# Kernel optimization log

Hardware: AMD Instinct MI355X
Metric: run time of the kernel (lower is better)

The kernel has to match this reference:

```python
import jax, jax.numpy as jnp
import numpy as np

LN_EPS = 1e-5


def _layernorm(x, w, b):
    mu = jnp.mean(x, axis=-1, keepdims=True)
    var = jnp.mean((x - mu) ** 2, axis=-1, keepdims=True)
    return (x - mu) * jax.lax.rsqrt(var + LN_EPS) * w + b


def setup_inputs() -> dict:
    key = jax.random.key(0)
    n, d = 512, 256
    ks = jax.random.split(key, 12)
    s = 1.0 / np.sqrt(d)
    inp = {
        "h": jax.random.normal(ks[0], (n, d), dtype=jnp.float32),
        "e": jax.random.normal(ks[1], (n, n, d), dtype=jnp.float32),
        "t_emb": jax.random.normal(ks[2], (d,), dtype=jnp.float32),
        "W1": jax.random.uniform(ks[3], (d, d), jnp.float32, -s, s),
        "W2": jax.random.uniform(ks[4], (d, d), jnp.float32, -s, s),
        "W3": jax.random.uniform(ks[5], (d, d), jnp.float32, -s, s),
        "W_t": jax.random.uniform(ks[6], (d, d), jnp.float32, -s, s),
        "W4": jax.random.uniform(ks[7], (d, d), jnp.float32, -s, s),
        "W5": jax.random.uniform(ks[8], (d, d), jnp.float32, -s, s),
        "gate_w": jax.random.uniform(ks[9], (d, 1), jnp.float32, -s, s),
        "gate_b": jax.random.uniform(ks[10], (1,), jnp.float32, -s, s),
        "ln_e_w": jnp.ones((d,), jnp.float32),
        "ln_e_b": jnp.zeros((d,), jnp.float32),
        "ln_h_w": jnp.ones((d,), jnp.float32),
        "ln_h_b": jnp.zeros((d,), jnp.float32),
    }
    return inp


def reference(h, e, t_emb, W1, W2, W3, W_t, W4, W5, gate_w, gate_b,
              ln_e_w, ln_e_b, ln_h_w, ln_h_b):
    # nn.Linear applies x @ W.T (no bias except gate)
    t_bias = t_emb @ W_t.T                      # (d,)
    hi = (h @ W1.T)[:, None, :]                 # (n,1,d)
    hj = (h @ W2.T)[None, :, :]                 # (1,n,d)
    pre = hi + hj + jnp.einsum('ijd,kd->ijk', e, W3) + t_bias  # (n,n,d)
    e_new = jax.nn.relu(_layernorm(pre, ln_e_w, ln_e_b))       # (n,n,d)
    logits = e_new @ gate_w + gate_b            # (n,n,1)
    eta = jax.nn.softmax(logits, axis=1)        # softmax over j (dim=1)
    agg = jnp.einsum('ijk,ijd,kd->ik', eta * 1.0, e_new, W5) if False else \
          jnp.sum(eta * jnp.einsum('ijd,kd->ijk', e_new, W5), axis=1)  # (n,d)
    h_new = h + jax.nn.relu(_layernorm(h @ W4.T + agg, ln_h_w, ln_h_b))
    return (h_new, e_new)
```

## Files before the change

kernel.cpp:

```cpp
#include <hip/hip_runtime.h>

#define NN 512
#define DD 256

typedef float f32x4 __attribute__((ext_vector_type(4)));
typedef short s16x8 __attribute__((ext_vector_type(8)));

__device__ __forceinline__ unsigned short f2bf(float f) {
    unsigned u = __float_as_uint(f);
    u += 0x7fffu + ((u >> 16) & 1u);
    return (unsigned short)(u >> 16);
}

__global__ __launch_bounds__(256) void k1_pre(
    const float* __restrict__ h,  const float* __restrict__ W1,
    const float* __restrict__ W2, const float* __restrict__ W4,
    const float* __restrict__ t_emb, const float* __restrict__ W_t,
    const float* __restrict__ W3,
    float* __restrict__ hW1, float* __restrict__ hW2, float* __restrict__ hW4,
    float* __restrict__ tbias, unsigned short* __restrict__ w3b)
{
    __shared__ float xs[8][DD];
    const int b = blockIdx.x;
    const int t = threadIdx.x;
    if (b < 64) {
        #pragma unroll
        for (int r = 0; r < 8; ++r) xs[r][t] = h[(size_t)(b * 8 + r) * DD + t];
        __syncthreads();
        float a1[8], a2[8], a4[8];
        #pragma unroll
        for (int r = 0; r < 8; ++r) { a1[r] = 0.f; a2[r] = 0.f; a4[r] = 0.f; }
        for (int d = 0; d < DD; ++d) {
            const float w1 = W1[(size_t)t * DD + d];
            const float w2 = W2[(size_t)t * DD + d];
            const float w4 = W4[(size_t)t * DD + d];
            #pragma unroll
            for (int r = 0; r < 8; ++r) {
                const float x = xs[r][d];
                a1[r] = fmaf(x, w1, a1[r]);
                a2[r] = fmaf(x, w2, a2[r]);
                a4[r] = fmaf(x, w4, a4[r]);
            }
        }
        #pragma unroll
        for (int r = 0; r < 8; ++r) {
            const size_t o = (size_t)(b * 8 + r) * DD + t;
            hW1[o] = a1[r]; hW2[o] = a2[r]; hW4[o] = a4[r];
        }
    } else {
        xs[0][t] = t_emb[t];
        __syncthreads();
        float a = 0.f;
        for (int d = 0; d < DD; ++d) a = fmaf(xs[0][d], W_t[(size_t)t * DD + d], a);
        tbias[t] = a;
        for (int c = t; c < DD * DD / 4; c += 256) {
            const f32x4 v = *reinterpret_cast<const f32x4*>(W3 + (size_t)c * 4);
            const unsigned lo = ((unsigned)f2bf(v[1]) << 16) | f2bf(v[0]);
            const unsigned hi = ((unsigned)f2bf(v[3]) << 16) | f2bf(v[2]);
            *reinterpret_cast<uint2*>(w3b + (size_t)c * 4) = make_uint2(lo, hi);
        }
    }
}

__global__ __launch_bounds__(256) void k2_big(
    const float* __restrict__ e,
    const unsigned short* __restrict__ w3b,
    const float* __restrict__ hW1, const float* __restrict__ hW2,
    const float* __restrict__ tbias,
    const float* __restrict__ gate_w, const float* __restrict__ gate_b,
    const float* __restrict__ ln_e_w, const float* __restrict__ ln_e_b,
    float* __restrict__ out_e, float* __restrict__ logits)
{
    const int blk = blockIdx.x;
    const int row_base = blk * 64;
    const int i = row_base >> 9;
    const int tid = threadIdx.x;
    const int w = tid >> 6;
    const int l = tid & 63;
    const int l15 = l & 15;
    const int lg = l >> 4;

    __shared__ __align__(16) unsigned char sA[64 * 256 * 2];
    __shared__ float s_part[64][4][2];
    __shared__ float s_mu[64];
    __shared__ float s_rs[64];
    __shared__ float s_glog[64][4];

    {
        const float* src = e + (size_t)row_base * DD;
        #pragma unroll
        for (int s = 0; s < 16; ++s) {
            const int flat = s * 256 + tid;
            const int r = flat >> 6;
            const int c4 = (flat & 63) * 4;
            const f32x4 v = *reinterpret_cast<const f32x4*>(src + (size_t)flat * 4);
            const unsigned lo = ((unsigned)f2bf(v[1]) << 16) | f2bf(v[0]);
            const unsigned hi = ((unsigned)f2bf(v[3]) << 16) | f2bf(v[2]);
            const unsigned byte = ((unsigned)(r * 512 + c4 * 2)) ^ ((unsigned)(r & 7) << 4);
            *reinterpret_cast<uint2*>(sA + byte) = make_uint2(lo, hi);
        }
    }
    __syncthreads();

    f32x4 acc[4][4];
    #pragma unroll
    for (int m = 0; m < 4; ++m)
        #pragma unroll
        for (int n = 0; n < 4; ++n)
            acc[m][n] = (f32x4){0.f, 0.f, 0.f, 0.f};

    const unsigned aswz = ((unsigned)(l15 & 7) << 4);
    for (int kk = 0; kk < 8; ++kk) {
        s16x8 afr[4];
        #pragma unroll
        for (int m = 0; m < 4; ++m) {
            const unsigned byte = ((unsigned)((m * 16 + l15) * 512 + kk * 64 + lg * 16)) ^ aswz;
            afr[m] = *reinterpret_cast<const s16x8*>(sA + byte);
        }
        #pragma unroll
        for (int n = 0; n < 4; ++n) {
            const int col = w * 64 + n * 16 + l15;
            const s16x8 bfr = *reinterpret_cast<const s16x8*>(w3b + (size_t)col * DD + kk * 32 + lg * 8);
            #pragma unroll
            for (int m = 0; m < 4; ++m)
                acc[m][n] = __builtin_amdgcn_mfma_f32_16x16x32_bf16(afr[m], bfr, acc[m][n], 0, 0, 0);
        }
    }

    float hw1c[4], tbc[4], lnwc[4], lnbc[4], gwc[4];
    #pragma unroll
    for (int n = 0; n < 4; ++n) {
        const int col = w * 64 + n * 16 + l15;
        hw1c[n] = hW1[(size_t)i * DD + col];
        tbc[n]  = tbias[col];
        lnwc[n] = ln_e_w[col];
        lnbc[n] = ln_e_b[col];
        gwc[n]  = gate_w[col];
    }

    #pragma unroll
    for (int m = 0; m < 4; ++m) {
        #pragma unroll
        for (int q = 0; q < 4; ++q) {
            const int r = m * 16 + lg * 4 + q;
            const int j = (row_base + r) & 511;
            float s1 = 0.f, s2 = 0.f;
            #pragma unroll
            for (int n = 0; n < 4; ++n) {
                const int col = w * 64 + n * 16 + l15;
                float v = acc[m][n][q] + hw1c[n] + tbc[n] + hW2[(size_t)j * DD + col];
                acc[m][n][q] = v;
                s1 += v;
                s2 += v * v;
            }
            #pragma unroll
            for (int s = 1; s < 16; s <<= 1) {
                s1 += __shfl_xor(s1, s, 64);
                s2 += __shfl_xor(s2, s, 64);
            }
            if (l15 == 0) { s_part[r][w][0] = s1; s_part[r][w][1] = s2; }
        }
    }
    __syncthreads();
    if (tid < 64) {
        float S1 = 0.f, S2 = 0.f;
        #pragma unroll
        for (int ww = 0; ww < 4; ++ww) { S1 += s_part[tid][ww][0]; S2 += s_part[tid][ww][1]; }
        const float mu = S1 * (1.f / 256.f);
        const float var = S2 * (1.f / 256.f) - mu * mu;
        s_mu[tid] = mu;
        s_rs[tid] = rsqrtf(var + 1e-5f);
    }
    __syncthreads();

    #pragma unroll
    for (int m = 0; m < 4; ++m) {
        #pragma unroll
        for (int q = 0; q < 4; ++q) {
            const int r = m * 16 + lg * 4 + q;
            const float mu = s_mu[r];
            const float rs = s_rs[r];
            const size_t rowg = (size_t)(row_base + r);
            float gl = 0.f;
            #pragma unroll
            for (int n = 0; n < 4; ++n) {
                const int col = w * 64 + n * 16 + l15;
                float v = (acc[m][n][q] - mu) * rs * lnwc[n] + lnbc[n];
                v = fmaxf(v, 0.f);
                out_e[rowg * DD + col] = v;
                gl = fmaf(v, gwc[n], gl);
            }
            #pragma unroll
            for (int s = 1; s < 16; s <<= 1) gl += __shfl_xor(gl, s, 64);
            if (l15 == 0) s_glog[r][w] = gl;
        }
    }
    __syncthreads();
    if (tid < 64) {
        float g = gate_b[0];
        #pragma unroll
        for (int ww = 0; ww < 4; ++ww) g += s_glog[tid][ww];
        logits[(size_t)row_base + tid] = g;
    }
}

__global__ __launch_bounds__(256) void k3_soft(
    const float* __restrict__ logits, const float* __restrict__ out_e,
    float* __restrict__ weighted)
{
    const int i = blockIdx.x;
    const int t = threadIdx.x;
    const int w = t >> 6;
    const int l = t & 63;
    __shared__ float seta[NN];
    __shared__ float red[256];
    __shared__ float red2[4][DD];

    const float l0 = logits[(size_t)i * NN + t];
    const float l1 = logits[(size_t)i * NN + 256 + t];

    red[t] = fmaxf(l0, l1);
    __syncthreads();
    for (int s = 128; s > 0; s >>= 1) {
        if (t < s) red[t] = fmaxf(red[t], red[t + s]);
        __syncthreads();
    }
    const float mx = red[0];
    __syncthreads();

    const float e0 = expf(l0 - mx);
    const float e1 = expf(l1 - mx);
    red[t] = e0 + e1;
    __syncthreads();
    for (int s = 128; s > 0; s >>= 1) {
        if (t < s) red[t] += red[t + s];
        __syncthreads();
    }
    const float inv = 1.f / red[0];
    seta[t] = e0 * inv;
    seta[256 + t] = e1 * inv;
    __syncthreads();

    const float* base = out_e + (size_t)i * NN * DD;
    f32x4 a0 = (f32x4){0.f, 0.f, 0.f, 0.f};
    f32x4 a1v = (f32x4){0.f, 0.f, 0.f, 0.f};
    for (int j0 = 0; j0 < NN; j0 += 8) {
        const int ja = j0 + w;
        const int jb = j0 + 4 + w;
        const float ea = seta[ja];
        const float eb = seta[jb];
        const f32x4 va = *reinterpret_cast<const f32x4*>(base + (size_t)ja * DD + l * 4);
        const f32x4 vb = *reinterpret_cast<const f32x4*>(base + (size_t)jb * DD + l * 4);
        #pragma unroll
        for (int q = 0; q < 4; ++q) {
            a0[q] = fmaf(ea, va[q], a0[q]);
            a1v[q] = fmaf(eb, vb[q], a1v[q]);
        }
    }
    #pragma unroll
    for (int q = 0; q < 4; ++q) a0[q] += a1v[q];
    *reinterpret_cast<f32x4*>(&red2[w][l * 4]) = a0;
    __syncthreads();
    weighted[(size_t)i * DD + t] = red2[0][t] + red2[1][t] + red2[2][t] + red2[3][t];
}

__global__ __launch_bounds__(256) void k4_final(
    const float* __restrict__ weighted, const float* __restrict__ W5,
    const float* __restrict__ hW4, const float* __restrict__ h,
    const float* __restrict__ ln_h_w, const float* __restrict__ ln_h_b,
    float* __restrict__ out_h)
{
    const int i = blockIdx.x;
    const int k = threadIdx.x;
    __shared__ float xs[DD];
    __shared__ float red[256];

    xs[k] = weighted[(size_t)i * DD + k];
    __syncthreads();
    float a = 0.f;
    for (int d = 0; d < DD; ++d) a = fmaf(xs[d], W5[(size_t)k * DD + d], a);
    const float p = hW4[(size_t)i * DD + k] + a;

    red[k] = p;
    __syncthreads();
    for (int s = 128; s > 0; s >>= 1) {
        if (k < s) red[k] += red[k + s];
        __syncthreads();
    }
    const float mu = red[0] * (1.f / 256.f);
    __syncthreads();
    const float d0 = p - mu;
    red[k] = d0 * d0;
    __syncthreads();
    for (int s = 128; s > 0; s >>= 1) {
        if (k < s) red[k] += red[k + s];
        __syncthreads();
    }
    const float rs = rsqrtf(red[0] * (1.f / 256.f) + 1e-5f);
    float v = d0 * rs * ln_h_w[k] + ln_h_b[k];
    v = fmaxf(v, 0.f);
    out_h[(size_t)i * DD + k] = h[(size_t)i * DD + k] + v;
}

extern "C" void kernel_launch(void* const* d_in, const int* in_sizes, int n_in,
                              void* d_out, int out_size, void* d_ws, size_t ws_size,
                              hipStream_t stream)
{
    const float* h      = (const float*)d_in[0];
    const float* e      = (const float*)d_in[1];
    const float* t_emb  = (const float*)d_in[2];
    const float* W1     = (const float*)d_in[3];
    const float* W2     = (const float*)d_in[4];
    const float* W3     = (const float*)d_in[5];
    const float* W_t    = (const float*)d_in[6];
    const float* W4     = (const float*)d_in[7];
    const float* W5     = (const float*)d_in[8];
    const float* gate_w = (const float*)d_in[9];
    const float* gate_b = (const float*)d_in[10];
    const float* ln_e_w = (const float*)d_in[11];
    const float* ln_e_b = (const float*)d_in[12];
    const float* ln_h_w = (const float*)d_in[13];
    const float* ln_h_b = (const float*)d_in[14];

    float* out_h = (float*)d_out;
    float* out_e = out_h + NN * DD;

    float* wsf      = (float*)d_ws;
    float* hW1      = wsf;
    float* hW2      = hW1 + NN * DD;
    float* hW4      = hW2 + NN * DD;
    float* tbias    = hW4 + NN * DD;
    float* logits   = tbias + DD;
    float* weighted = logits + NN * NN;
    unsigned short* w3b = (unsigned short*)(weighted + NN * DD);

    k1_pre<<<65, 256, 0, stream>>>(h, W1, W2, W4, t_emb, W_t, W3,
                                   hW1, hW2, hW4, tbias, w3b);
    k2_big<<<4096, 256, 0, stream>>>(e, w3b, hW1, hW2, tbias, gate_w, gate_b,
                                     ln_e_w, ln_e_b, out_e, logits);
    k3_soft<<<512, 256, 0, stream>>>(logits, out_e, weighted);
    k4_final<<<512, 256, 0, stream>>>(weighted, W5, hW4, h, ln_h_w, ln_h_b, out_h);
}
```

Before: 326.1 us.

## Give each wave full rows in k2 to drop LDS staging and block syncs

The main edge kernel now gives each wave 16 complete rows across all 256 output columns. A operands are loaded from global straight into registers as bf16, and the LayerNorm and gate-logit reductions are done entirely with intra-wave shuffles. This removes the shared-memory A tile and the cross-wave partial-sum exchanges with their barriers, and adds a launch-bounds occupancy hint. The t_emb bias is folded into the hW1 precompute, so k2 reads one fewer vector. In exchange each wave now reads all of W3 (256x256 bf16) from global/L2 rather than a quarter of it, and register pressure rises with 16 accumulator tiles plus 8 A fragments.

```diff
diff --git a/kernel.cpp b/kernel.cpp
--- a/kernel.cpp
+++ b/kernel.cpp
@@ -17,23 +17,27 @@
     const float* __restrict__ W2, const float* __restrict__ W4,
     const float* __restrict__ t_emb, const float* __restrict__ W_t,
     const float* __restrict__ W3,
-    float* __restrict__ hW1, float* __restrict__ hW2, float* __restrict__ hW4,
-    float* __restrict__ tbias, unsigned short* __restrict__ w3b)
+    float* __restrict__ hb, float* __restrict__ hW2, float* __restrict__ hW4,
+    unsigned short* __restrict__ w3b)
 {
     __shared__ float xs[8][DD];
+    __shared__ float st[DD];
     const int b = blockIdx.x;
     const int t = threadIdx.x;
     if (b < 64) {
         #pragma unroll
         for (int r = 0; r < 8; ++r) xs[r][t] = h[(size_t)(b * 8 + r) * DD + t];
+        st[t] = t_emb[t];
         __syncthreads();
         float a1[8], a2[8], a4[8];
         #pragma unroll
         for (int r = 0; r < 8; ++r) { a1[r] = 0.f; a2[r] = 0.f; a4[r] = 0.f; }
+        float tb = 0.f;
         for (int d = 0; d < DD; ++d) {
             const float w1 = W1[(size_t)t * DD + d];
             const float w2 = W2[(size_t)t * DD + d];
             const float w4 = W4[(size_t)t * DD + d];
+            tb = fmaf(st[d], W_t[(size_t)t * DD + d], tb);
             #pragma unroll
             for (int r = 0; r < 8; ++r) {
                 const float x = xs[r][d];
@@ -45,14 +49,9 @@
         #pragma unroll
         for (int r = 0; r < 8; ++r) {
             const size_t o = (size_t)(b * 8 + r) * DD + t;
-            hW1[o] = a1[r]; hW2[o] = a2[r]; hW4[o] = a4[r];
+            hb[o] = a1[r] + tb; hW2[o] = a2[r]; hW4[o] = a4[r];
         }
     } else {
-        xs[0][t] = t_emb[t];
-        __syncthreads();
-        float a = 0.f;
-        for (int d = 0; d < DD; ++d) a = fmaf(xs[0][d], W_t[(size_t)t * DD + d], a);
-        tbias[t] = a;
         for (int c = t; c < DD * DD / 4; c += 256) {
             const f32x4 v = *reinterpret_cast<const f32x4*>(W3 + (size_t)c * 4);
             const unsigned lo = ((unsigned)f2bf(v[1]) << 16) | f2bf(v[0]);
@@ -62,145 +61,99 @@
     }
 }
 
-__global__ __launch_bounds__(256) void k2_big(
+__global__ __launch_bounds__(256, 3) void k2_big(
     const float* __restrict__ e,
     const unsigned short* __restrict__ w3b,
-    const float* __restrict__ hW1, const float* __restrict__ hW2,
-    const float* __restrict__ tbias,
+    const float* __restrict__ hb, const float* __restrict__ hW2,
     const float* __restrict__ gate_w, const float* __restrict__ gate_b,
     const float* __restrict__ ln_e_w, const float* __restrict__ ln_e_b,
     float* __restrict__ out_e, float* __restrict__ logits)
 {
-    const int blk = blockIdx.x;
-    const int row_base = blk * 64;
+    const int row_base = blockIdx.x * 64;
     const int i = row_base >> 9;
     const int tid = threadIdx.x;
     const int w = tid >> 6;
     const int l = tid & 63;
     const int l15 = l & 15;
     const int lg = l >> 4;
-
-    __shared__ __align__(16) unsigned char sA[64 * 256 * 2];
-    __shared__ float s_part[64][4][2];
-    __shared__ float s_mu[64];
-    __shared__ float s_rs[64];
-    __shared__ float s_glog[64][4];
-
-    {
-        const float* src = e + (size_t)row_base * DD;
-        #pragma unroll
-        for (int s = 0; s < 16; ++s) {
-            const int flat = s * 256 + tid;
-            const int r = flat >> 6;
-            const int c4 = (flat & 63) * 4;
-            const f32x4 v = *reinterpret_cast<const f32x4*>(src + (size_t)flat * 4);
-            const unsigned lo = ((unsigned)f2bf(v[1]) << 16) | f2bf(v[0]);
-            const unsigned hi = ((unsigned)f2bf(v[3]) << 16) | f2bf(v[2]);
-            const unsigned byte = ((unsigned)(r * 512 + c4 * 2)) ^ ((unsigned)(r & 7) << 4);
-            *reinterpret_cast<uint2*>(sA + byte) = make_uint2(lo, hi);
-        }
-    }
-    __syncthreads();
-
-    f32x4 acc[4][4];
-    #pragma unroll
-    for (int m = 0; m < 4; ++m)
-        #pragma unroll
-        for (int n = 0; n < 4; ++n)
-            acc[m][n] = (f32x4){0.f, 0.f, 0.f, 0.f};
-
-    const unsigned aswz = ((unsigned)(l15 & 7) << 4);
+    const int g0 = row_base + w * 16;
+
+    const float* arow = e + (size_t)(g0 + l15) * DD + lg * 8;
+    s16x8 abf[8];
+    #pragma unroll
     for (int kk = 0; kk < 8; ++kk) {
-        s16x8 afr[4];
-        #pragma unroll
-        for (int m = 0; m < 4; ++m) {
-            const unsigned byte = ((unsigned)((m * 16 + l15) * 512 + kk * 64 + lg * 16)) ^ aswz;
-            afr[m] = *reinterpret_cast<const s16x8*>(sA + byte);
-        }
-        #pragma unroll
-        for (int n = 0; n < 4; ++n) {
-            const int col = w * 64 + n * 16 + l15;
-            const s16x8 bfr = *reinterpret_cast<const s16x8*>(w3b + (size_t)col * DD + kk * 32 + lg * 8);
-            #pragma unroll
-            for (int m = 0; m < 4; ++m)
-                acc[m][n] = __builtin_amdgcn_mfma_f32_16x16x32_bf16(afr[m], bfr, acc[m][n], 0, 0, 0);
-        }
-    }
-
-    float hw1c[4], tbc[4], lnwc[4], lnbc[4], gwc[4];
-    #pragma unroll
-    for (int n = 0; n < 4; ++n) {
-        const int col = w * 64 + n * 16 + l15;
-        hw1c[n] = hW1[(size_t)i * DD + col];
-        tbc[n]  = tbias[col];
-        lnwc[n] = ln_e_w[col];
-        lnbc[n] = ln_e_b[col];
-        gwc[n]  = gate_w[col];
-    }
-
-    #pragma unroll
-    for (int m = 0; m < 4; ++m) {
+        const f32x4 v0 = *reinterpret_cast<const f32x4*>(arow + kk * 32);
+        const f32x4 v1 = *reinterpret_cast<const f32x4*>(arow + kk * 32 + 4);
+        s16x8 a;
+        a[0] = (short)f2bf(v0[0]); a[1] = (short)f2bf(v0[1]);
+        a[2] = (short)f2bf(v0[2]); a[3] = (short)f2bf(v0[3]);
+        a[4] = (short)f2bf(v1[0]); a[5] = (short)f2bf(v1[1]);
+        a[6] = (short)f2bf(v1[2]); a[7] = (short)f2bf(v1[3]);
+        abf[kk] = a;
+    }
+
+    f32x4 acc[16];
+    #pragma unroll
+    for (int n = 0; n < 16; ++n) acc[n] = (f32x4){0.f, 0.f, 0.f, 0.f};
+
+    const unsigned short* bp = w3b + (size_t)l15 * DD + lg * 8;
+    #pragma unroll
+    for (int kk = 0; kk < 8; ++kk) {
+        #pragma unroll
+        for (int n = 0; n < 16; ++n) {
+            const s16x8 bfr = *reinterpret_cast<const s16x8*>(bp + (size_t)n * 16 * DD + kk * 32);
+            acc[n] = __builtin_amdgcn_mfma_f32_16x16x32_bf16(abf[kk], bfr, acc[n], 0, 0, 0);
+        }
+    }
+
+    float hbn[16];
+    #pragma unroll
+    for (int n = 0; n < 16; ++n) hbn[n] = hb[(size_t)i * DD + n * 16 + l15];
+
+    float mu4[4], rs4[4];
+    #pragma unroll
+    for (int q = 0; q < 4; ++q) {
+        const int jrow = (g0 + lg * 4 + q) & 511;
+        const float* h2p = hW2 + (size_t)jrow * DD + l15;
+        float s1 = 0.f, s2 = 0.f;
+        #pragma unroll
+        for (int n = 0; n < 16; ++n) {
+            float v = acc[n][q] + hbn[n] + h2p[n * 16];
+            acc[n][q] = v;
+            s1 += v;
+            s2 = fmaf(v, v, s2);
+        }
+        #pragma unroll
+        for (int s = 1; s < 16; s <<= 1) {
+            s1 += __shfl_xor(s1, s, 64);
+            s2 += __shfl_xor(s2, s, 64);
+        }
+        const float mu = s1 * (1.f / 256.f);
+        mu4[q] = mu;
+        rs4[q] = rsqrtf(s2 * (1.f / 256.f) - mu * mu + 1e-5f);
+    }
+
+    float gl[4] = {0.f, 0.f, 0.f, 0.f};
+    #pragma unroll
+    for (int n = 0; n < 16; ++n) {
+        const int col = n * 16 + l15;
+        const float lw = ln_e_w[col];
+        const float lb = ln_e_b[col];
+        const float gw = gate_w[col];
         #pragma unroll
         for (int q = 0; q < 4; ++q) {
-            const int r = m * 16 + lg * 4 + q;
-            const int j = (row_base + r) & 511;
-            float s1 = 0.f, s2 = 0.f;
-            #pragma unroll
-            for (int n = 0; n < 4; ++n) {
-                const int col = w * 64 + n * 16 + l15;
-                float v = acc[m][n][q] + hw1c[n] + tbc[n] + hW2[(size_t)j * DD + col];
-                acc[m][n][q] = v;
-                s1 += v;
-                s2 += v * v;
-            }
-            #pragma unroll
-            for (int s = 1; s < 16; s <<= 1) {
-                s1 += __shfl_xor(s1, s, 64);
-                s2 += __shfl_xor(s2, s, 64);
-            }
-            if (l15 == 0) { s_part[r][w][0] = s1; s_part[r][w][1] = s2; }
-        }
-    }
-    __syncthreads();
-    if (tid < 64) {
-        float S1 = 0.f, S2 = 0.f;
-        #pragma unroll
-        for (int ww = 0; ww < 4; ++ww) { S1 += s_part[tid][ww][0]; S2 += s_part[tid][ww][1]; }
-        const float mu = S1 * (1.f / 256.f);
-        const float var = S2 * (1.f / 256.f) - mu * mu;
-        s_mu[tid] = mu;
-        s_rs[tid] = rsqrtf(var + 1e-5f);
-    }
-    __syncthreads();
-
-    #pragma unroll
-    for (int m = 0; m < 4; ++m) {
-        #pragma unroll
-        for (int q = 0; q < 4; ++q) {
-            const int r = m * 16 + lg * 4 + q;
-            const float mu = s_mu[r];
-            const float rs = s_rs[r];
-            const size_t rowg = (size_t)(row_base + r);
-            float gl = 0.f;
-            #pragma unroll
-            for (int n = 0; n < 4; ++n) {
-                const int col = w * 64 + n * 16 + l15;
-                float v = (acc[m][n][q] - mu) * rs * lnwc[n] + lnbc[n];
-                v = fmaxf(v, 0.f);
-                out_e[rowg * DD + col] = v;
-                gl = fmaf(v, gwc[n], gl);
-            }
-            #pragma unroll
-            for (int s = 1; s < 16; s <<= 1) gl += __shfl_xor(gl, s, 64);
-            if (l15 == 0) s_glog[r][w] = gl;
-        }
-    }
-    __syncthreads();
-    if (tid < 64) {
-        float g = gate_b[0];
-        #pragma unroll
-        for (int ww = 0; ww < 4; ++ww) g += s_glog[tid][ww];
-        logits[(size_t)row_base + tid] = g;
+            float v = (acc[n][q] - mu4[q]) * rs4[q] * lw + lb;
+            v = fmaxf(v, 0.f);
+            out_e[(size_t)(g0 + lg * 4 + q) * DD + col] = v;
+            gl[q] = fmaf(v, gw, gl[q]);
+        }
+    }
+    const float gb = gate_b[0];
+    #pragma unroll
+    for (int q = 0; q < 4; ++q) {
+        #pragma unroll
+        for (int s = 1; s < 16; s <<= 1) gl[q] += __shfl_xor(gl[q], s, 64);
+        if (l15 == 0) logits[(size_t)(g0 + lg * 4 + q)] = gl[q] + gb;
     }
 }
 
@@ -326,17 +279,16 @@
     float* out_e = out_h + NN * DD;
 
     float* wsf      = (float*)d_ws;
-    float* hW1      = wsf;
-    float* hW2      = hW1 + NN * DD;
+    float* hb       = wsf;
+    float* hW2      = hb + NN * DD;
     float* hW4      = hW2 + NN * DD;
-    float* tbias    = hW4 + NN * DD;
-    float* logits   = tbias + DD;
+    float* logits   = hW4 + NN * DD;
     float* weighted = logits + NN * NN;
     unsigned short* w3b = (unsigned short*)(weighted + NN * DD);
 
     k1_pre<<<65, 256, 0, stream>>>(h, W1, W2, W4, t_emb, W_t, W3,
-                                   hW1, hW2, hW4, tbias, w3b);
-    k2_big<<<4096, 256, 0, stream>>>(e, w3b, hW1, hW2, tbias, gate_w, gate_b,
+                                   hb, hW2, hW4, w3b);
+    k2_big<<<4096, 256, 0, stream>>>(e, w3b, hb, hW2, gate_w, gate_b,
                                      ln_e_w, ln_e_b, out_e, logits);
     k3_soft<<<512, 256, 0, stream>>>(logits, out_e, weighted);
     k4_final<<<512, 256, 0, stream>>>(weighted, W5, hW4, h, ln_h_w, ln_h_b, out_h);
```

Result: slower. 453.0 us (+38.9%).

## Halve k2 row tile, prefetch B fragments, fold time bias into hW1

Applied to the files above, without the earlier changes.

The main edge kernel now handles 32 rows per block instead of 64, launching twice as many blocks with half the shared memory and accumulator registers, which should raise occupancy. Global loads of e are issued into registers before the W3 fragments are fetched, and W3 fragments are double-buffered across the k loop so the next step's loads overlap the MFMAs. The time-embedding bias is folded into hW1 in the first kernel, removing one workspace array and one load per column. The cost is that each block reuses its W3 fragments over fewer rows, so more W3 traffic per row.

```diff
diff --git a/kernel.cpp b/kernel.cpp
--- a/kernel.cpp
+++ b/kernel.cpp
@@ -17,23 +17,27 @@
     const float* __restrict__ W2, const float* __restrict__ W4,
     const float* __restrict__ t_emb, const float* __restrict__ W_t,
     const float* __restrict__ W3,
-    float* __restrict__ hW1, float* __restrict__ hW2, float* __restrict__ hW4,
-    float* __restrict__ tbias, unsigned short* __restrict__ w3b)
+    float* __restrict__ hb, float* __restrict__ hW2, float* __restrict__ hW4,
+    unsigned short* __restrict__ w3b)
 {
     __shared__ float xs[8][DD];
+    __shared__ float st[DD];
     const int b = blockIdx.x;
     const int t = threadIdx.x;
     if (b < 64) {
         #pragma unroll
         for (int r = 0; r < 8; ++r) xs[r][t] = h[(size_t)(b * 8 + r) * DD + t];
+        st[t] = t_emb[t];
         __syncthreads();
         float a1[8], a2[8], a4[8];
         #pragma unroll
         for (int r = 0; r < 8; ++r) { a1[r] = 0.f; a2[r] = 0.f; a4[r] = 0.f; }
+        float tb = 0.f;
         for (int d = 0; d < DD; ++d) {
             const float w1 = W1[(size_t)t * DD + d];
             const float w2 = W2[(size_t)t * DD + d];
             const float w4 = W4[(size_t)t * DD + d];
+            tb = fmaf(st[d], W_t[(size_t)t * DD + d], tb);
             #pragma unroll
             for (int r = 0; r < 8; ++r) {
                 const float x = xs[r][d];
@@ -45,14 +49,9 @@
         #pragma unroll
         for (int r = 0; r < 8; ++r) {
             const size_t o = (size_t)(b * 8 + r) * DD + t;
-            hW1[o] = a1[r]; hW2[o] = a2[r]; hW4[o] = a4[r];
+            hb[o] = a1[r] + tb; hW2[o] = a2[r]; hW4[o] = a4[r];
         }
     } else {
-        xs[0][t] = t_emb[t];
-        __syncthreads();
-        float a = 0.f;
-        for (int d = 0; d < DD; ++d) a = fmaf(xs[0][d], W_t[(size_t)t * DD + d], a);
-        tbias[t] = a;
         for (int c = t; c < DD * DD / 4; c += 256) {
             const f32x4 v = *reinterpret_cast<const f32x4*>(W3 + (size_t)c * 4);
             const unsigned lo = ((unsigned)f2bf(v[1]) << 16) | f2bf(v[0]);
@@ -65,14 +64,12 @@
 __global__ __launch_bounds__(256) void k2_big(
     const float* __restrict__ e,
     const unsigned short* __restrict__ w3b,
-    const float* __restrict__ hW1, const float* __restrict__ hW2,
-    const float* __restrict__ tbias,
+    const float* __restrict__ hb, const float* __restrict__ hW2,
     const float* __restrict__ gate_w, const float* __restrict__ gate_b,
     const float* __restrict__ ln_e_w, const float* __restrict__ ln_e_b,
     float* __restrict__ out_e, float* __restrict__ logits)
 {
-    const int blk = blockIdx.x;
-    const int row_base = blk * 64;
+    const int row_base = blockIdx.x * 32;
     const int i = row_base >> 9;
     const int tid = threadIdx.x;
     const int w = tid >> 6;
@@ -80,78 +77,94 @@
     const int l15 = l & 15;
     const int lg = l >> 4;
 
-    __shared__ __align__(16) unsigned char sA[64 * 256 * 2];
-    __shared__ float s_part[64][4][2];
-    __shared__ float s_mu[64];
-    __shared__ float s_rs[64];
-    __shared__ float s_glog[64][4];
-
-    {
-        const float* src = e + (size_t)row_base * DD;
-        #pragma unroll
-        for (int s = 0; s < 16; ++s) {
-            const int flat = s * 256 + tid;
-            const int r = flat >> 6;
-            const int c4 = (flat & 63) * 4;
-            const f32x4 v = *reinterpret_cast<const f32x4*>(src + (size_t)flat * 4);
-            const unsigned lo = ((unsigned)f2bf(v[1]) << 16) | f2bf(v[0]);
-            const unsigned hi = ((unsigned)f2bf(v[3]) << 16) | f2bf(v[2]);
-            const unsigned byte = ((unsigned)(r * 512 + c4 * 2)) ^ ((unsigned)(r & 7) << 4);
-            *reinterpret_cast<uint2*>(sA + byte) = make_uint2(lo, hi);
-        }
-    }
-    __syncthreads();
-
-    f32x4 acc[4][4];
-    #pragma unroll
-    for (int m = 0; m < 4; ++m)
+    __shared__ __align__(16) unsigned char sA[32 * 256 * 2];
+    __shared__ float s_part[32][4][2];
+    __shared__ float s_mu[32];
+    __shared__ float s_rs[32];
+    __shared__ float s_glog[32][4];
+
+    const float* src = e + (size_t)row_base * DD;
+    f32x4 av[8];
+    #pragma unroll
+    for (int s = 0; s < 8; ++s)
+        av[s] = *reinterpret_cast<const f32x4*>(src + (size_t)(s * 256 + tid) * 4);
+
+    const unsigned short* bp = w3b + (size_t)(w * 64 + l15) * DD + lg * 8;
+    s16x8 bcur[4];
+    #pragma unroll
+    for (int n = 0; n < 4; ++n)
+        bcur[n] = *reinterpret_cast<const s16x8*>(bp + (size_t)n * 16 * DD);
+
+    #pragma unroll
+    for (int s = 0; s < 8; ++s) {
+        const int flat = s * 256 + tid;
+        const int r = flat >> 6;
+        const int c4 = (flat & 63) * 4;
+        const f32x4 v = av[s];
+        const unsigned lo = ((unsigned)f2bf(v[1]) << 16) | f2bf(v[0]);
+        const unsigned hi = ((unsigned)f2bf(v[3]) << 16) | f2bf(v[2]);
+        const unsigned byte = ((unsigned)(r * 512 + c4 * 2)) ^ ((unsigned)(r & 7) << 4);
+        *reinterpret_cast<uint2*>(sA + byte) = make_uint2(lo, hi);
+    }
+    __syncthreads();
+
+    f32x4 acc[2][4];
+    #pragma unroll
+    for (int m = 0; m < 2; ++m)
         #pragma unroll
         for (int n = 0; n < 4; ++n)
             acc[m][n] = (f32x4){0.f, 0.f, 0.f, 0.f};
 
     const unsigned aswz = ((unsigned)(l15 & 7) << 4);
+    #pragma unroll
     for (int kk = 0; kk < 8; ++kk) {
-        s16x8 afr[4];
-        #pragma unroll
-        for (int m = 0; m < 4; ++m) {
+        s16x8 bnxt[4];
+        if (kk < 7) {
+            #pragma unroll
+            for (int n = 0; n < 4; ++n)
+                bnxt[n] = *reinterpret_cast<const s16x8*>(bp + (size_t)n * 16 * DD + (kk + 1) * 32);
+        }
+        s16x8 afr[2];
+        #pragma unroll
+        for (int m = 0; m < 2; ++m) {
             const unsigned byte = ((unsigned)((m * 16 + l15) * 512 + kk * 64 + lg * 16)) ^ aswz;
             afr[m] = *reinterpret_cast<const s16x8*>(sA + byte);
         }
         #pragma unroll
-        for (int n = 0; n < 4; ++n) {
-            const int col = w * 64 + n * 16 + l15;
-            const s16x8 bfr = *reinterpret_cast<const s16x8*>(w3b + (size_t)col * DD + kk * 32 + lg * 8);
-            #pragma unroll
-            for (int m = 0; m < 4; ++m)
-                acc[m][n] = __builtin_amdgcn_mfma_f32_16x16x32_bf16(afr[m], bfr, acc[m][n], 0, 0, 0);
-        }
-    }
-
-    float hw1c[4], tbc[4], lnwc[4], lnbc[4], gwc[4];
+        for (int n = 0; n < 4; ++n)
+            #pragma unroll
+            for (int m = 0; m < 2; ++m)
+                acc[m][n] = __builtin_amdgcn_mfma_f32_16x16x32_bf16(afr[m], bcur[n], acc[m][n], 0, 0, 0);
+        if (kk < 7) {
+            #pragma unroll
+            for (int n = 0; n < 4; ++n) bcur[n] = bnxt[n];
+        }
+    }
+
+    float hbn[4], lnwc[4], lnbc[4], gwc[4];
     #pragma unroll
     for (int n = 0; n < 4; ++n) {
         const int col = w * 64 + n * 16 + l15;
-        hw1c[n] = hW1[(size_t)i * DD + col];
-        tbc[n]  = tbias[col];
+        hbn[n]  = hb[(size_t)i * DD + col];
         lnwc[n] = ln_e_w[col];
         lnbc[n] = ln_e_b[col];
         gwc[n]  = gate_w[col];
     }
 
     #pragma unroll
-    for (int m = 0; m < 4; ++m) {
+    for (int m = 0; m < 2; ++m) {
         #pragma unroll
         for (int q = 0; q < 4; ++q) {
             const int r = m * 16 + lg * 4 + q;
             const int j = (row_base + r) & 511;
+            const float* h2p = hW2 + (size_t)j * DD + w * 64 + l15;
             float s1 = 0.f, s2 = 0.f;
             #pragma unroll
             for (int n = 0; n < 4; ++n) {
-                const int col = w * 64 + n * 16 + l15;
-                float v = acc[m][n][q] + hw1c[n] + tbc[n] + hW2[(size_t)j * DD + col];
+                float v = acc[m][n][q] + hbn[n] + h2p[n * 16];
                 acc[m][n][q] = v;
                 s1 += v;
-                s2 += v * v;
+                s2 = fmaf(v, v, s2);
             }
             #pragma unroll
             for (int s = 1; s < 16; s <<= 1) {
@@ -162,7 +175,7 @@
         }
     }
     __syncthreads();
-    if (tid < 64) {
+    if (tid < 32) {
         float S1 = 0.f, S2 = 0.f;
         #pragma unroll
         for (int ww = 0; ww < 4; ++ww) { S1 += s_part[tid][ww][0]; S2 += s_part[tid][ww][1]; }
@@ -174,7 +187,7 @@
     __syncthreads();
 
     #pragma unroll
-    for (int m = 0; m < 4; ++m) {
+    for (int m = 0; m < 2; ++m) {
         #pragma unroll
         for (int q = 0; q < 4; ++q) {
             const int r = m * 16 + lg * 4 + q;
@@ -196,7 +209,7 @@
         }
     }
     __syncthreads();
-    if (tid < 64) {
+    if (tid < 32) {
         float g = gate_b[0];
         #pragma unroll
         for (int ww = 0; ww < 4; ++ww) g += s_glog[tid][ww];
@@ -326,17 +339,16 @@
     float* out_e = out_h + NN * DD;
 
     float* wsf      = (float*)d_ws;
-    float* hW1      = wsf;
-    float* hW2      = hW1 + NN * DD;
+    float* hb       = wsf;
+    float* hW2      = hb + NN * DD;
     float* hW4      = hW2 + NN * DD;
-    float* tbias    = hW4 + NN * DD;
-    float* logits   = tbias + DD;
+    float* logits   = hW4 + NN * DD;
     float* weighted = logits + NN * NN;
     unsigned short* w3b = (unsigned short*)(weighted + NN * DD);
 
     k1_pre<<<65, 256, 0, stream>>>(h, W1, W2, W4, t_emb, W_t, W3,
-                                   hW1, hW2, hW4, tbias, w3b);
-    k2_big<<<4096, 256, 0, stream>>>(e, w3b, hW1, hW2, tbias, gate_w, gate_b,
+                                   hb, hW2, hW4, w3b);
+    k2_big<<<8192, 256, 0, stream>>>(e, w3b, hb, hW2, gate_w, gate_b,
                                      ln_e_w, ln_e_b, out_e, logits);
     k3_soft<<<512, 256, 0, stream>>>(logits, out_e, weighted);
     k4_final<<<512, 256, 0, stream>>>(weighted, W5, hW4, h, ln_h_w, ln_h_b, out_h);
```

Measured after the change: 325.4 us. About the same (-0.2%).
